# Kernel tuning notes

Measured on AMD Instinct MI355X. Metric: run time of the kernel, lower is better.

Reference implementation:

```python
import jax, jax.numpy as jnp
import numpy as np

DIM = 256
CTX_DIM = 256
HEADS = 32
DIM_HEAD = 32
INNER = HEADS * DIM_HEAD


def mish(x):
    return x * jnp.tanh(jax.nn.softplus(x))


def setup_inputs() -> dict:
    key = jax.random.key(0)
    ks = jax.random.split(key, 16)
    B, Lq, Lp = 16, 128, 512
    s = 0.02
    return {
        "x": jax.random.normal(ks[0], (B * Lq, DIM), jnp.float32),
        "context": jax.random.normal(ks[1], (B * Lp, CTX_DIM), jnp.float32),
        "batch_dis": jax.random.normal(ks[2], (B, Lp, Lq, 3), jnp.float32),
        "batch_dis_emb": jax.random.normal(ks[3], (B, Lp, Lq, HEADS), jnp.float32),
        "protein_len": Lp,
        "ligand_len": Lq,
        # params ([in, out] layout, torch Linear transposed)
        "W_qk": jax.random.normal(ks[4], (DIM, INNER), jnp.float32) * s,
        "W_v": jax.random.normal(ks[5], (DIM, INNER), jnp.float32) * s,
        "W_cqk": jax.random.normal(ks[6], (CTX_DIM, INNER), jnp.float32) * s,
        "W_cv": jax.random.normal(ks[7], (CTX_DIM, INNER), jnp.float32) * s,
        "W_m1": jax.random.normal(ks[8], (2 * HEADS, 4 * HEADS), jnp.float32) * s,
        "W_m2": jax.random.normal(ks[9], (4 * HEADS, 2 * HEADS), jnp.float32) * s,
        "b_m2": jnp.zeros((2 * HEADS,), jnp.float32),
        "W_o": jax.random.normal(ks[10], (INNER, DIM), jnp.float32) * s,
        "b_o": jnp.zeros((DIM,), jnp.float32),
        "W_d1": jax.random.normal(ks[11], (HEADS, 2 * HEADS), jnp.float32) * s,
        "b_d1": jnp.zeros((2 * HEADS,), jnp.float32),
        "W_d2": jax.random.normal(ks[12], (2 * HEADS, HEADS), jnp.float32) * s,
        "b_d2": jnp.zeros((HEADS,), jnp.float32),
    }


def reference(x, context, batch_dis, batch_dis_emb, protein_len, ligand_len,
              W_qk, W_v, W_cqk, W_cv, W_m1, W_m2, b_m2, W_o, b_o,
              W_d1, b_d1, W_d2, b_d2):
    h, dh = HEADS, DIM_HEAD
    scale = dh ** -0.5
    B = x.shape[0] // ligand_len
    # projections; split heads: [B, L, h, dh]
    qk = (x @ W_qk).reshape(B, ligand_len, h, dh)
    cqk = (context @ W_cqk).reshape(B, protein_len, h, dh)
    cv = (context @ W_cv).reshape(B, protein_len, h, dh)
    # ligand->protein attention scores: [B, h, Lq, Lp]
    sim = jnp.einsum('bihd,bjhd->bhij', qk, cqk) * scale
    # distance-embedding channels: [B, Lp, Lq, h] -> [B, h, Lq, Lp]
    dis = jnp.transpose(batch_dis_emb, (0, 3, 2, 1))
    s = jnp.concatenate([sim, dis], axis=1)           # [B, 2h, Lq, Lp]
    s = jnp.moveaxis(s, 1, -1)                        # [B, Lq, Lp, 2h]
    s = mish(s @ W_m1) @ W_m2 + b_m2                  # attn_mlp over channel dim
    attn = jax.nn.softmax(s, axis=2)                  # softmax over protein (j)
    # first h heads attend into context values
    out = jnp.einsum('bijh,bjhd->bihd', attn[..., :h], cv)
    out = out.reshape(B * ligand_len, h * dh) @ W_o + b_o   # [N_lig, dim]
    # last h heads aggregate 3D distance vectors
    out_dis = jnp.einsum('bijh,bjid->bidh', attn[..., h:], batch_dis)
    out_dis = out_dis.reshape(B * ligand_len, 3, h)
    out_dis = mish(out_dis @ W_d1 + b_d1) @ W_d2 + b_d2      # [N_lig, 3, h]
    return out, out_dis
```

## Files before the change

### kernel.cpp

```cpp
#include <hip/hip_runtime.h>

typedef unsigned short u16;
typedef unsigned int   u32;
typedef __attribute__((ext_vector_type(8))) short bf16x8;
typedef __attribute__((ext_vector_type(4))) float f32x4;

#define MFMA_BF16 __builtin_amdgcn_mfma_f32_16x16x32_bf16

__device__ __forceinline__ float bf2f(u16 v) {
    u32 x = ((u32)v) << 16;
    return __builtin_bit_cast(float, x);
}
__device__ __forceinline__ float bflo(u32 u) { return __builtin_bit_cast(float, u << 16); }
__device__ __forceinline__ float bfhi(u32 u) { return __builtin_bit_cast(float, u & 0xffff0000u); }
__device__ __forceinline__ u16 f2bf(float f) {
    u32 x = __builtin_bit_cast(u32, f);
    u32 r = (x + 0x7fffu + ((x >> 16) & 1u)) >> 16;
    return (u16)r;
}
__device__ __forceinline__ float mishf(float x) {
    float p = 1.f + __expf(x);
    float q = p * p;
    float r = (q - 1.f) / (q + 1.f);
    return (x > 20.f) ? x : x * r;
}

__global__ __launch_bounds__(256) void gemm_mfma(
    const float* __restrict__ A, const float* __restrict__ W, u16* __restrict__ C,
    int M, int N, int K, float scale)
{
    __shared__ u16 As[128 * 40];
    __shared__ u16 Bf[4 * 64 * 8];

    const int tid = threadIdx.x;
    const int lane = tid & 63, wv = tid >> 6;
    const int qd = lane >> 4, ln = lane & 15;
    const int m0 = blockIdx.y * 128, n0 = blockIdx.x * 64;

    f32x4 acc[2][4];
#pragma unroll
    for (int a = 0; a < 2; ++a)
#pragma unroll
        for (int nt = 0; nt < 4; ++nt) acc[a][nt] = (f32x4){0.f, 0.f, 0.f, 0.f};

    for (int k0 = 0; k0 < K; k0 += 32) {
        {
            int r = tid >> 1, kh = (tid & 1) * 16;
            const float* ap = A + (size_t)(m0 + r) * K + k0 + kh;
            float4 a0 = ((const float4*)ap)[0];
            float4 a1 = ((const float4*)ap)[1];
            float4 a2 = ((const float4*)ap)[2];
            float4 a3 = ((const float4*)ap)[3];
            uint4 p0, p1;
            p0.x = (u32)f2bf(a0.x) | ((u32)f2bf(a0.y) << 16);
            p0.y = (u32)f2bf(a0.z) | ((u32)f2bf(a0.w) << 16);
            p0.z = (u32)f2bf(a1.x) | ((u32)f2bf(a1.y) << 16);
            p0.w = (u32)f2bf(a1.z) | ((u32)f2bf(a1.w) << 16);
            p1.x = (u32)f2bf(a2.x) | ((u32)f2bf(a2.y) << 16);
            p1.y = (u32)f2bf(a2.z) | ((u32)f2bf(a2.w) << 16);
            p1.z = (u32)f2bf(a3.x) | ((u32)f2bf(a3.y) << 16);
            p1.w = (u32)f2bf(a3.z) | ((u32)f2bf(a3.w) << 16);
            *(uint4*)&As[r * 40 + kh]     = p0;
            *(uint4*)&As[r * 40 + kh + 8] = p1;
        }
        {
            int nt = tid >> 6, q = (tid >> 4) & 3, nn = tid & 15;
            const float* wp = W + (size_t)(k0 + q * 8) * N + n0 + nt * 16 + nn;
            bf16x8 v;
#pragma unroll
            for (int j = 0; j < 8; ++j) v[j] = (short)f2bf(wp[(size_t)j * N]);
            *(bf16x8*)&Bf[tid * 8] = v;
        }
        __syncthreads();
        bf16x8 af0 = *(const bf16x8*)&As[(wv * 32 + ln) * 40 + qd * 8];
        bf16x8 af1 = *(const bf16x8*)&As[(wv * 32 + 16 + ln) * 40 + qd * 8];
#pragma unroll
        for (int nt = 0; nt < 4; ++nt) {
            bf16x8 bfr = *(const bf16x8*)&Bf[(nt * 64 + lane) * 8];
            acc[0][nt] = MFMA_BF16(af0, bfr, acc[0][nt], 0, 0, 0);
            acc[1][nt] = MFMA_BF16(af1, bfr, acc[1][nt], 0, 0, 0);
        }
        __syncthreads();
    }
#pragma unroll
    for (int a = 0; a < 2; ++a)
#pragma unroll
        for (int nt = 0; nt < 4; ++nt)
#pragma unroll
            for (int r = 0; r < 4; ++r)
                C[(size_t)(m0 + wv * 32 + a * 16 + qd * 4 + r) * N + n0 + nt * 16 + ln] =
                    f2bf(acc[a][nt][r] * scale);
}

__global__ __launch_bounds__(256) void transpose_cv(
    const u16* __restrict__ cv, u16* __restrict__ cvT)
{
    __shared__ u16 T[64 * 80];
    const int tid = threadIdx.x;
    const int ct = blockIdx.x * 64, jt = blockIdx.y * 64, b = blockIdx.z;
    {
        int j_l = tid >> 2, seg = tid & 3;
        const u16* src = cv + (size_t)(b * 512 + jt + j_l) * 1024 + ct + seg * 16;
        uint4 v0 = ((const uint4*)src)[0];
        uint4 v1 = ((const uint4*)src)[1];
        u16* tp = &T[seg * 16 * 80 + j_l];
        tp[0*80] = (u16)(v0.x & 0xffff); tp[1*80] = (u16)(v0.x >> 16);
        tp[2*80] = (u16)(v0.y & 0xffff); tp[3*80] = (u16)(v0.y >> 16);
        tp[4*80] = (u16)(v0.z & 0xffff); tp[5*80] = (u16)(v0.z >> 16);
        tp[6*80] = (u16)(v0.w & 0xffff); tp[7*80] = (u16)(v0.w >> 16);
        tp[8*80] = (u16)(v1.x & 0xffff); tp[9*80] = (u16)(v1.x >> 16);
        tp[10*80] = (u16)(v1.y & 0xffff); tp[11*80] = (u16)(v1.y >> 16);
        tp[12*80] = (u16)(v1.z & 0xffff); tp[13*80] = (u16)(v1.z >> 16);
        tp[14*80] = (u16)(v1.w & 0xffff); tp[15*80] = (u16)(v1.w >> 16);
    }
    __syncthreads();
    {
        int ch_l = tid >> 2, sg = tid & 3;
        u16* dst = cvT + (size_t)(b * 1024 + ct + ch_l) * 512 + jt + sg * 16;
        ((uint4*)dst)[0] = *(const uint4*)&T[ch_l * 80 + sg * 16];
        ((uint4*)dst)[1] = *(const uint4*)&T[ch_l * 80 + sg * 16 + 8];
    }
}

__global__ __launch_bounds__(256) void prep(
    const float* __restrict__ Wo, const float* __restrict__ W1, const float* __restrict__ W2,
    u16* __restrict__ WoT, u16* __restrict__ w1b, u16* __restrict__ w2b)
{
    const int bb = blockIdx.x, t = threadIdx.x;
    if (bb < 256) {
#pragma unroll
        for (int kk = 0; kk < 4; ++kk)
            WoT[(size_t)t * 1024 + bb * 4 + kk] = f2bf(Wo[(size_t)(bb * 4 + kk) * 256 + t]);
    } else {
        for (int u = 0; u < 32; ++u) {
            int idx = t + 256 * u;
            int j = idx & 7, lane = (idx >> 3) & 63, f = idx >> 9;
            int n = lane & 15, q = lane >> 4, ntc = f & 7, ks = f >> 3;
            w1b[idx] = f2bf(W1[(ks * 32 + q * 8 + j) * 128 + ntc * 16 + n]);
        }
        for (int u = 0; u < 32; ++u) {
            int idx = t + 256 * u;
            int j = idx & 7, lane = (idx >> 3) & 63, f = idx >> 9;
            int n = lane & 15, q = lane >> 4, ot = f & 3, ks = f >> 2;
            w2b[idx] = f2bf(W2[(ks * 32 + q * 8 + j) * 64 + ot * 16 + n]);
        }
    }
}

__global__ __launch_bounds__(256, 1) void attn5(
    const u16* __restrict__ qk,
    const u16* __restrict__ cqk,
    const u16* __restrict__ cvT,
    const float* __restrict__ bde,
    const float* __restrict__ bdis,
    const u16* __restrict__ w1b, const u16* __restrict__ w2b,
    const float* __restrict__ b2,
    float* __restrict__ partial)
{
    __shared__ __align__(16) char smem[62976];
    u16*   ES  = (u16*)smem;
    u16*   MT  = (u16*)(smem + 20480);
    float* BD  = (float*)(smem + 25600);
    u16*   EST = (u16*)(smem + 29696);
    u16*   W1B = (u16*)(smem + 54784);

    const int tid = threadIdx.x;
    const int lane = tid & 63, wv = tid >> 6;
    const int qd = lane >> 4, ln = lane & 15;
    const int nblk = blockIdx.x;
    const int xcd = nblk & 7, g = nblk >> 3;
    const int b = xcd * 2 + (g & 1);
    const int r2 = g >> 1;
    const int it = r2 >> 2, jq = r2 & 3;
    const int i0 = it * 16;
    const int pidx = (b * 8 + it) * 4 + jq;

    for (int k = tid; k < 4096; k += 256) ((u32*)W1B)[k] = ((const u32*)w1b)[k];

    float b2r[4];
#pragma unroll
    for (int ot = 0; ot < 4; ++ot) b2r[ot] = b2[ot * 16 + ln];

    bf16x8 qkf[8];
#pragma unroll
    for (int hh = 0; hh < 8; ++hh) {
        int h = wv * 8 + hh;
        qkf[hh] = *(const bf16x8*)(qk + ((size_t)(b * 128 + i0 + ln)) * 1024 + h * 32 + qd * 8);
    }

    f32x4 oacc[8][2];
#pragma unroll
    for (int a = 0; a < 8; ++a)
#pragma unroll
        for (int c = 0; c < 2; ++c) oacc[a][c] = (f32x4){0.f, 0.f, 0.f, 0.f};
    float dn[4][4] = {};
    float dd[4][3][2] = {};

    __syncthreads();

#pragma clang loop unroll(disable)
    for (int ps = 0; ps < 8; ++ps) {
        const int jg0 = jq * 128 + ps * 16;

        {
            const u16* crow = cqk + (size_t)(b * 512 + jg0 + ln) * 1024 + qd * 8;
#pragma unroll
            for (int hh = 0; hh < 4; ++hh) {
                const int h0 = wv * 8 + hh * 2;
                bf16x8 b0 = *(const bf16x8*)(crow + h0 * 32);
                bf16x8 b1 = *(const bf16x8*)(crow + (h0 + 1) * 32);
                f32x4 c0 = (f32x4){0.f, 0.f, 0.f, 0.f}, c1 = c0;
                c0 = MFMA_BF16(qkf[hh * 2],     b0, c0, 0, 0, 0);
                c1 = MFMA_BF16(qkf[hh * 2 + 1], b1, c1, 0, 0, 0);
#pragma unroll
                for (int r = 0; r < 4; ++r) {
                    u32 pv = (u32)f2bf(c0[r]) | ((u32)f2bf(c1[r]) << 16);
                    *(u32*)&ES[((qd * 4 + r) * 16 + ln) * 40 + h0] = pv;
                }
            }
        }
        {
            int ii = tid & 15, jj = tid >> 4;
            const float* sp = bdis + ((size_t)(b * 512 + jg0 + jj) * 128 + i0 + ii) * 3;
            float* dp2 = &BD[(ii * 16 + jj) * 4];
            dp2[0] = sp[0]; dp2[1] = sp[1]; dp2[2] = sp[2];
        }
        __syncthreads();

#pragma unroll
        for (int s = 0; s < 4; ++s) {
            const int i_loc = wv * 4 + s;
            bf16x8 af0 = *(const bf16x8*)&ES[(i_loc * 16 + ln) * 40 + qd * 8];
            bf16x8 af1;
            {
                const float* dp = bde + (((size_t)(b * 512 + jg0 + ln)) * 128 + i0 + i_loc) * 32 + qd * 8;
                float4 a0 = ((const float4*)dp)[0];
                float4 a1 = ((const float4*)dp)[1];
                af1[0] = (short)f2bf(a0.x); af1[1] = (short)f2bf(a0.y);
                af1[2] = (short)f2bf(a0.z); af1[3] = (short)f2bf(a0.w);
                af1[4] = (short)f2bf(a1.x); af1[5] = (short)f2bf(a1.y);
                af1[6] = (short)f2bf(a1.z); af1[7] = (short)f2bf(a1.w);
            }
            f32x4 uacc[4];
#pragma unroll
            for (int ot = 0; ot < 4; ++ot) uacc[ot] = (f32x4){0.f, 0.f, 0.f, 0.f};
            u16* mt = MT + wv * 640;
#pragma unroll
            for (int cg = 0; cg < 4; ++cg) {
                bf16x8 w00 = *(const bf16x8*)&W1B[((cg * 2 + 0) * 64 + lane) * 8];
                bf16x8 w01 = *(const bf16x8*)&W1B[((cg * 2 + 1) * 64 + lane) * 8];
                bf16x8 w10 = *(const bf16x8*)&W1B[((8 + cg * 2 + 0) * 64 + lane) * 8];
                bf16x8 w11 = *(const bf16x8*)&W1B[((8 + cg * 2 + 1) * 64 + lane) * 8];
                f32x4 t0 = (f32x4){0.f, 0.f, 0.f, 0.f}, t1 = t0;
                t0 = MFMA_BF16(af0, w00, t0, 0, 0, 0);
                t0 = MFMA_BF16(af1, w10, t0, 0, 0, 0);
                t1 = MFMA_BF16(af0, w01, t1, 0, 0, 0);
                t1 = MFMA_BF16(af1, w11, t1, 0, 0, 0);
#pragma unroll
                for (int r = 0; r < 4; ++r) {
                    mt[(qd * 4 + r) * 40 + ln]      = f2bf(mishf(t0[r]));
                    mt[(qd * 4 + r) * 40 + 16 + ln] = f2bf(mishf(t1[r]));
                }
                bf16x8 ta = *(const bf16x8*)&mt[ln * 40 + qd * 8];
#pragma unroll
                for (int ot = 0; ot < 4; ++ot) {
                    bf16x8 wf = *(const bf16x8*)(w2b + ((size_t)(cg * 4 + ot) * 64 + lane) * 8);
                    uacc[ot] = MFMA_BF16(ta, wf, uacc[ot], 0, 0, 0);
                }
            }
            float Ev[4][4];
#pragma unroll
            for (int ot = 0; ot < 4; ++ot) {
#pragma unroll
                for (int r = 0; r < 4; ++r) Ev[ot][r] = __expf(uacc[ot][r] + b2r[ot]);
                dn[s][ot] += Ev[ot][0] + Ev[ot][1] + Ev[ot][2] + Ev[ot][3];
            }
#pragma unroll
            for (int r = 0; r < 4; ++r) {
                const float* bp = &BD[(i_loc * 16 + qd * 4 + r) * 4];
#pragma unroll
                for (int d = 0; d < 3; ++d) {
                    dd[s][d][0] += Ev[2][r] * bp[d];
                    dd[s][d][1] += Ev[3][r] * bp[d];
                }
            }
#pragma unroll
            for (int ot = 0; ot < 2; ++ot) {
                const int base = (ot * 16 + ln) * 392 + i_loc * 24 + qd * 4;
                *(u32*)&EST[base]     = (u32)f2bf(Ev[ot][0]) | ((u32)f2bf(Ev[ot][1]) << 16);
                *(u32*)&EST[base + 2] = (u32)f2bf(Ev[ot][2]) | ((u32)f2bf(Ev[ot][3]) << 16);
            }
        }
        __syncthreads();

#pragma unroll
        for (int hh = 0; hh < 8; ++hh) {
            const int h = wv * 8 + hh;
            bf16x8 af = (bf16x8){0, 0, 0, 0, 0, 0, 0, 0};
            if (qd < 2) af = *(const bf16x8*)&EST[h * 392 + ln * 24 + qd * 8];
#pragma unroll
            for (int nt = 0; nt < 2; ++nt) {
                bf16x8 bfr = (bf16x8){0, 0, 0, 0, 0, 0, 0, 0};
                if (qd < 2)
                    bfr = *(const bf16x8*)(cvT + ((size_t)(b * 1024 + h * 32 + nt * 16 + ln)) * 512 + jg0 + qd * 8);
                oacc[hh][nt] = MFMA_BF16(af, bfr, oacc[hh][nt], 0, 0, 0);
            }
        }
        __syncthreads();
    }

    float* P = partial + (size_t)pidx * 18944;
#pragma unroll
    for (int hh = 0; hh < 8; ++hh)
#pragma unroll
        for (int nt = 0; nt < 2; ++nt)
#pragma unroll
            for (int r = 0; r < 4; ++r)
                P[(size_t)(qd * 4 + r) * 1024 + (wv * 8 + hh) * 32 + nt * 16 + ln] = oacc[hh][nt][r];
#pragma unroll
    for (int s = 0; s < 4; ++s)
#pragma unroll
        for (int ot = 0; ot < 4; ++ot) {
            float v = dn[s][ot];
            v += __shfl_xor(v, 16, 64);
            v += __shfl_xor(v, 32, 64);
            if (qd == 0) P[16384 + (wv * 4 + s) * 64 + ot * 16 + ln] = v;
        }
#pragma unroll
    for (int s = 0; s < 4; ++s)
#pragma unroll
        for (int d = 0; d < 3; ++d)
#pragma unroll
            for (int o = 0; o < 2; ++o) {
                float v = dd[s][d][o];
                v += __shfl_xor(v, 16, 64);
                v += __shfl_xor(v, 32, 64);
                if (qd == 0) P[17408 + (wv * 4 + s) * 96 + d * 32 + o * 16 + ln] = v;
            }
}

__global__ __launch_bounds__(256, 2) void finalize(
    const float* __restrict__ partial, const u16* __restrict__ WoT,
    const float* __restrict__ bo,
    const float* __restrict__ Wd1, const float* __restrict__ bd1,
    const float* __restrict__ Wd2, const float* __restrict__ bd2,
    float* __restrict__ out0, float* __restrict__ out1)
{
    __shared__ float denomL[1024];
    __shared__ u16 preL[16 * 1032];
    __shared__ float odisL[1536];
    __shared__ float r1L[3072];

    const int tid = threadIdx.x;
    const int f = blockIdx.x;
    const int b = f >> 3, it = f & 7;
    const int row0 = b * 128 + it * 16;
    const float* P0 = partial + (size_t)(f * 4 + 0) * 18944;
    const float* P1 = partial + (size_t)(f * 4 + 1) * 18944;
    const float* P2 = partial + (size_t)(f * 4 + 2) * 18944;
    const float* P3 = partial + (size_t)(f * 4 + 3) * 18944;

    for (int k = tid; k < 1024; k += 256)
        denomL[k] = P0[16384 + k] + P1[16384 + k] + P2[16384 + k] + P3[16384 + k];
    __syncthreads();

    {
        const int h = tid >> 3;
#pragma unroll
        for (int i = 0; i < 16; ++i) {
            float4 a = *(const float4*)&P0[(size_t)i * 1024 + tid * 4];
            float4 bq = *(const float4*)&P1[(size_t)i * 1024 + tid * 4];
            float4 c = *(const float4*)&P2[(size_t)i * 1024 + tid * 4];
            float4 d = *(const float4*)&P3[(size_t)i * 1024 + tid * 4];
            float rdn = 1.f / denomL[i * 64 + h];
            u32 p0 = (u32)f2bf((a.x + bq.x + c.x + d.x) * rdn) | ((u32)f2bf((a.y + bq.y + c.y + d.y) * rdn) << 16);
            u32 p1 = (u32)f2bf((a.z + bq.z + c.z + d.z) * rdn) | ((u32)f2bf((a.w + bq.w + c.w + d.w) * rdn) << 16);
            *(uint2*)(void*)&preL[i * 1032 + tid * 4] = make_uint2(p0, p1);
        }
    }
    for (int idx = tid; idx < 1536; idx += 256) {
        int i = idx / 96, rm = idx % 96, h = rm & 31;
        odisL[idx] = (P0[17408 + idx] + P1[17408 + idx] + P2[17408 + idx] + P3[17408 + idx])
                     / denomL[i * 64 + 32 + h];
    }
    __syncthreads();

    {
        const int lane = tid & 63, wv = tid >> 6;
        const int qd = lane >> 4, ln = lane & 15;
        f32x4 acc[4];
#pragma unroll
        for (int nt = 0; nt < 4; ++nt) acc[nt] = (f32x4){0.f, 0.f, 0.f, 0.f};
#pragma clang loop unroll(disable)
        for (int ks = 0; ks < 32; ++ks) {
            bf16x8 af = *(const bf16x8*)&preL[ln * 1032 + ks * 32 + qd * 8];
#pragma unroll
            for (int nt = 0; nt < 4; ++nt) {
                bf16x8 wf = *(const bf16x8*)(WoT + ((size_t)(wv * 64 + nt * 16 + ln)) * 1024 + ks * 32 + qd * 8);
                acc[nt] = MFMA_BF16(af, wf, acc[nt], 0, 0, 0);
            }
        }
#pragma unroll
        for (int nt = 0; nt < 4; ++nt) {
            int col = wv * 64 + nt * 16 + ln;
            float bv = bo[col];
#pragma unroll
            for (int r = 0; r < 4; ++r)
                out0[(size_t)(row0 + qd * 4 + r) * 256 + col] = acc[nt][r] + bv;
        }
    }

    for (int idx = tid; idx < 3072; idx += 256) {
        int i = idx / 192, rm = idx % 192, d = rm / 64, c = rm & 63;
        float t = bd1[c];
#pragma unroll
        for (int hh = 0; hh < 32; ++hh)
            t += odisL[i * 96 + d * 32 + hh] * Wd1[hh * 64 + c];
        r1L[idx] = mishf(t);
    }
    __syncthreads();
    for (int idx = tid; idx < 1536; idx += 256) {
        int i = idx / 96, rm = idx % 96, d = rm >> 5, h = rm & 31;
        float v = bd2[h];
#pragma unroll
        for (int c = 0; c < 64; ++c)
            v += r1L[i * 192 + d * 64 + c] * Wd2[c * 32 + h];
        out1[(size_t)(row0 + i) * 96 + d * 32 + h] = v;
    }
}

extern "C" void kernel_launch(void* const* d_in, const int* in_sizes, int n_in,
                              void* d_out, int out_size, void* d_ws, size_t ws_size,
                              hipStream_t stream) {
    const float* x    = (const float*)d_in[0];
    const float* ctx  = (const float*)d_in[1];
    const float* bdis = (const float*)d_in[2];
    const float* bde  = (const float*)d_in[3];
    const float* Wqk  = (const float*)d_in[6];
    const float* Wcqk = (const float*)d_in[8];
    const float* Wcv  = (const float*)d_in[9];
    const float* Wm1  = (const float*)d_in[10];
    const float* Wm2  = (const float*)d_in[11];
    const float* bm2  = (const float*)d_in[12];
    const float* Wo   = (const float*)d_in[13];
    const float* bo   = (const float*)d_in[14];
    const float* Wd1  = (const float*)d_in[15];
    const float* bd1  = (const float*)d_in[16];
    const float* Wd2  = (const float*)d_in[17];
    const float* bd2  = (const float*)d_in[18];

    char* ws = (char*)d_ws;
    u16* qk_ws  = (u16*)(ws);
    u16* cqk_ws = (u16*)(ws + 4194304);
    u16* cvT_ws = (u16*)(ws + 20971520);
    u16* w1b    = (u16*)(ws + 37748736);
    u16* w2b    = (u16*)(ws + 37765120);
    u16* WoT    = (u16*)(ws + 37781504);
    float* part = (float*)(ws + 38305792);
    u16* cv_rm  = (u16*)(ws + 38305792);

    float* out0 = (float*)d_out;
    float* out1 = out0 + (size_t)2048 * 256;

    const float SCALE = 0.17677669529663687f;

    prep<<<257, 256, 0, stream>>>(Wo, Wm1, Wm2, WoT, w1b, w2b);
    gemm_mfma<<<dim3(16, 16), 256, 0, stream>>>(x,   Wqk,  qk_ws,  2048, 1024, 256, SCALE);
    gemm_mfma<<<dim3(16, 64), 256, 0, stream>>>(ctx, Wcqk, cqk_ws, 8192, 1024, 256, 1.0f);
    gemm_mfma<<<dim3(16, 64), 256, 0, stream>>>(ctx, Wcv,  cv_rm,  8192, 1024, 256, 1.0f);
    transpose_cv<<<dim3(16, 8, 16), 256, 0, stream>>>(cv_rm, cvT_ws);
    attn5<<<512, 256, 0, stream>>>(qk_ws, cqk_ws, cvT_ws, bde, bdis, w1b, w2b, bm2, part);
    finalize<<<128, 256, 0, stream>>>(part, WoT, bo, Wd1, bd1, Wd2, bd2, out0, out1);
}
```

Measured before the change: 562.5 us.

## Use packed bf16 conversion and exp2 intrinsics with log2e folded into weights

Replaces the software round-to-nearest bf16 conversion with the hardware v_cvt_pk_bf16_f32 instruction across the GEMM, attention and reduction kernels. Mish is rewritten with raw v_exp_f32 and v_rcp_f32 plus FMAs in place of the division. The log2e factor is folded into W2 and b2 so the softmax exponent becomes a single exp2, and W2's channel order is permuted so mish outputs can be written as packed pairs. Distance loads move to float4 shared-memory accesses. The aim is fewer ALU instructions in the VALU-heavy attention loop, at the cost of dropping the x>20 guard in mish, which could overflow to inf/NaN for large inputs.

Result: slower. 577.3 us (+2.6%).

```diff
diff --git a/kernel.cpp b/kernel.cpp
--- a/kernel.cpp
+++ b/kernel.cpp
@@ -6,23 +6,34 @@
 typedef __attribute__((ext_vector_type(4))) float f32x4;
 
 #define MFMA_BF16 __builtin_amdgcn_mfma_f32_16x16x32_bf16
-
-__device__ __forceinline__ float bf2f(u16 v) {
-    u32 x = ((u32)v) << 16;
-    return __builtin_bit_cast(float, x);
-}
-__device__ __forceinline__ float bflo(u32 u) { return __builtin_bit_cast(float, u << 16); }
-__device__ __forceinline__ float bfhi(u32 u) { return __builtin_bit_cast(float, u & 0xffff0000u); }
+#define LOG2E 1.4426950408889634f
+
 __device__ __forceinline__ u16 f2bf(float f) {
     u32 x = __builtin_bit_cast(u32, f);
     u32 r = (x + 0x7fffu + ((x >> 16) & 1u)) >> 16;
     return (u16)r;
 }
+__device__ __forceinline__ u32 cvt_pk_bf16(float lo, float hi) {
+    u32 r;
+    asm("v_cvt_pk_bf16_f32 %0, %1, %2" : "=v"(r) : "v"(lo), "v"(hi));
+    return r;
+}
+__device__ __forceinline__ float exp2_asm(float x) {
+    float r;
+    asm("v_exp_f32 %0, %1" : "=v"(r) : "v"(x));
+    return r;
+}
+__device__ __forceinline__ float rcp_asm(float x) {
+    float r;
+    asm("v_rcp_f32 %0, %1" : "=v"(r) : "v"(x));
+    return r;
+}
 __device__ __forceinline__ float mishf(float x) {
-    float p = 1.f + __expf(x);
-    float q = p * p;
-    float r = (q - 1.f) / (q + 1.f);
-    return (x > 20.f) ? x : x * r;
+    float e = exp2_asm(x * LOG2E);
+    float p = 1.f + e;
+    float d = __builtin_fmaf(p, p, 1.f);
+    float r = __builtin_fmaf(-2.f, rcp_asm(d), 1.f);
+    return x * r;
 }
 
 __global__ __launch_bounds__(256) void gemm_mfma(
@@ -52,24 +63,28 @@
             float4 a2 = ((const float4*)ap)[2];
             float4 a3 = ((const float4*)ap)[3];
             uint4 p0, p1;
-            p0.x = (u32)f2bf(a0.x) | ((u32)f2bf(a0.y) << 16);
-            p0.y = (u32)f2bf(a0.z) | ((u32)f2bf(a0.w) << 16);
-            p0.z = (u32)f2bf(a1.x) | ((u32)f2bf(a1.y) << 16);
-            p0.w = (u32)f2bf(a1.z) | ((u32)f2bf(a1.w) << 16);
-            p1.x = (u32)f2bf(a2.x) | ((u32)f2bf(a2.y) << 16);
-            p1.y = (u32)f2bf(a2.z) | ((u32)f2bf(a2.w) << 16);
-            p1.z = (u32)f2bf(a3.x) | ((u32)f2bf(a3.y) << 16);
-            p1.w = (u32)f2bf(a3.z) | ((u32)f2bf(a3.w) << 16);
+            p0.x = cvt_pk_bf16(a0.x, a0.y);
+            p0.y = cvt_pk_bf16(a0.z, a0.w);
+            p0.z = cvt_pk_bf16(a1.x, a1.y);
+            p0.w = cvt_pk_bf16(a1.z, a1.w);
+            p1.x = cvt_pk_bf16(a2.x, a2.y);
+            p1.y = cvt_pk_bf16(a2.z, a2.w);
+            p1.z = cvt_pk_bf16(a3.x, a3.y);
+            p1.w = cvt_pk_bf16(a3.z, a3.w);
             *(uint4*)&As[r * 40 + kh]     = p0;
             *(uint4*)&As[r * 40 + kh + 8] = p1;
         }
         {
             int nt = tid >> 6, q = (tid >> 4) & 3, nn = tid & 15;
             const float* wp = W + (size_t)(k0 + q * 8) * N + n0 + nt * 16 + nn;
-            bf16x8 v;
-#pragma unroll
-            for (int j = 0; j < 8; ++j) v[j] = (short)f2bf(wp[(size_t)j * N]);
-            *(bf16x8*)&Bf[tid * 8] = v;
+            float w0 = wp[0], w1 = wp[(size_t)1 * N], w2 = wp[(size_t)2 * N], w3 = wp[(size_t)3 * N];
+            float w4 = wp[(size_t)4 * N], w5 = wp[(size_t)5 * N], w6 = wp[(size_t)6 * N], w7 = wp[(size_t)7 * N];
+            uint4 u;
+            u.x = cvt_pk_bf16(w0, w1);
+            u.y = cvt_pk_bf16(w2, w3);
+            u.z = cvt_pk_bf16(w4, w5);
+            u.w = cvt_pk_bf16(w6, w7);
+            *(uint4*)&Bf[tid * 8] = u;
         }
         __syncthreads();
         bf16x8 af0 = *(const bf16x8*)&As[(wv * 32 + ln) * 40 + qd * 8];
@@ -85,11 +100,15 @@
 #pragma unroll
     for (int a = 0; a < 2; ++a)
 #pragma unroll
-        for (int nt = 0; nt < 4; ++nt)
-#pragma unroll
-            for (int r = 0; r < 4; ++r)
-                C[(size_t)(m0 + wv * 32 + a * 16 + qd * 4 + r) * N + n0 + nt * 16 + ln] =
-                    f2bf(acc[a][nt][r] * scale);
+        for (int nt = 0; nt < 4; ++nt) {
+            u32 pk0 = cvt_pk_bf16(acc[a][nt][0] * scale, acc[a][nt][1] * scale);
+            u32 pk1 = cvt_pk_bf16(acc[a][nt][2] * scale, acc[a][nt][3] * scale);
+            size_t base = (size_t)(m0 + wv * 32 + a * 16 + qd * 4) * N + n0 + nt * 16 + ln;
+            C[base]               = (u16)pk0;
+            C[base + (size_t)N]   = (u16)(pk0 >> 16);
+            C[base + (size_t)2*N] = (u16)pk1;
+            C[base + (size_t)3*N] = (u16)(pk1 >> 16);
+        }
 }
 
 __global__ __launch_bounds__(256) void transpose_cv(
@@ -142,7 +161,9 @@
             int idx = t + 256 * u;
             int j = idx & 7, lane = (idx >> 3) & 63, f = idx >> 9;
             int n = lane & 15, q = lane >> 4, ot = f & 3, ks = f >> 2;
-            w2b[idx] = f2bf(W2[(ks * 32 + q * 8 + j) * 64 + ot * 16 + n]);
+            int k = q * 8 + j;
+            int ch = ((k & 1) << 4) | (k >> 1);
+            w2b[idx] = f2bf(W2[(ks * 32 + ch) * 64 + ot * 16 + n] * LOG2E);
         }
     }
 }
@@ -179,7 +200,7 @@
 
     float b2r[4];
 #pragma unroll
-    for (int ot = 0; ot < 4; ++ot) b2r[ot] = b2[ot * 16 + ln];
+    for (int ot = 0; ot < 4; ++ot) b2r[ot] = b2[ot * 16 + ln] * LOG2E;
 
     bf16x8 qkf[8];
 #pragma unroll
@@ -213,17 +234,16 @@
                 c0 = MFMA_BF16(qkf[hh * 2],     b0, c0, 0, 0, 0);
                 c1 = MFMA_BF16(qkf[hh * 2 + 1], b1, c1, 0, 0, 0);
 #pragma unroll
-                for (int r = 0; r < 4; ++r) {
-                    u32 pv = (u32)f2bf(c0[r]) | ((u32)f2bf(c1[r]) << 16);
-                    *(u32*)&ES[((qd * 4 + r) * 16 + ln) * 40 + h0] = pv;
-                }
+                for (int r = 0; r < 4; ++r)
+                    *(u32*)&ES[((qd * 4 + r) * 16 + ln) * 40 + h0] = cvt_pk_bf16(c0[r], c1[r]);
             }
         }
         {
             int ii = tid & 15, jj = tid >> 4;
             const float* sp = bdis + ((size_t)(b * 512 + jg0 + jj) * 128 + i0 + ii) * 3;
-            float* dp2 = &BD[(ii * 16 + jj) * 4];
-            dp2[0] = sp[0]; dp2[1] = sp[1]; dp2[2] = sp[2];
+            float4 v4;
+            v4.x = sp[0]; v4.y = sp[1]; v4.z = sp[2]; v4.w = 0.f;
+            *(float4*)&BD[(ii * 16 + jj) * 4] = v4;
         }
         __syncthreads();
 
@@ -236,10 +256,12 @@
                 const float* dp = bde + (((size_t)(b * 512 + jg0 + ln)) * 128 + i0 + i_loc) * 32 + qd * 8;
                 float4 a0 = ((const float4*)dp)[0];
                 float4 a1 = ((const float4*)dp)[1];
-                af1[0] = (short)f2bf(a0.x); af1[1] = (short)f2bf(a0.y);
-                af1[2] = (short)f2bf(a0.z); af1[3] = (short)f2bf(a0.w);
-                af1[4] = (short)f2bf(a1.x); af1[5] = (short)f2bf(a1.y);
-                af1[6] = (short)f2bf(a1.z); af1[7] = (short)f2bf(a1.w);
+                uint4 u;
+                u.x = cvt_pk_bf16(a0.x, a0.y);
+                u.y = cvt_pk_bf16(a0.z, a0.w);
+                u.z = cvt_pk_bf16(a1.x, a1.y);
+                u.w = cvt_pk_bf16(a1.z, a1.w);
+                af1 = __builtin_bit_cast(bf16x8, u);
             }
             f32x4 uacc[4];
 #pragma unroll
@@ -258,8 +280,8 @@
                 t1 = MFMA_BF16(af1, w11, t1, 0, 0, 0);
 #pragma unroll
                 for (int r = 0; r < 4; ++r) {
-                    mt[(qd * 4 + r) * 40 + ln]      = f2bf(mishf(t0[r]));
-                    mt[(qd * 4 + r) * 40 + 16 + ln] = f2bf(mishf(t1[r]));
+                    u32 pk = cvt_pk_bf16(mishf(t0[r]), mishf(t1[r]));
+                    *(u32*)&mt[(qd * 4 + r) * 40 + (ln << 1)] = pk;
                 }
                 bf16x8 ta = *(const bf16x8*)&mt[ln * 40 + qd * 8];
 #pragma unroll
@@ -272,23 +294,21 @@
 #pragma unroll
             for (int ot = 0; ot < 4; ++ot) {
 #pragma unroll
-                for (int r = 0; r < 4; ++r) Ev[ot][r] = __expf(uacc[ot][r] + b2r[ot]);
-                dn[s][ot] += Ev[ot][0] + Ev[ot][1] + Ev[ot][2] + Ev[ot][3];
+                for (int r = 0; r < 4; ++r) Ev[ot][r] = exp2_asm(uacc[ot][r] + b2r[ot]);
+                dn[s][ot] += (Ev[ot][0] + Ev[ot][1]) + (Ev[ot][2] + Ev[ot][3]);
             }
 #pragma unroll
             for (int r = 0; r < 4; ++r) {
-                const float* bp = &BD[(i_loc * 16 + qd * 4 + r) * 4];
-#pragma unroll
-                for (int d = 0; d < 3; ++d) {
-                    dd[s][d][0] += Ev[2][r] * bp[d];
-                    dd[s][d][1] += Ev[3][r] * bp[d];
-                }
+                float4 bp = *(const float4*)&BD[(i_loc * 16 + qd * 4 + r) * 4];
+                dd[s][0][0] += Ev[2][r] * bp.x; dd[s][0][1] += Ev[3][r] * bp.x;
+                dd[s][1][0] += Ev[2][r] * bp.y; dd[s][1][1] += Ev[3][r] * bp.y;
+                dd[s][2][0] += Ev[2][r] * bp.z; dd[s][2][1] += Ev[3][r] * bp.z;
             }
 #pragma unroll
             for (int ot = 0; ot < 2; ++ot) {
                 const int base = (ot * 16 + ln) * 392 + i_loc * 24 + qd * 4;
-                *(u32*)&EST[base]     = (u32)f2bf(Ev[ot][0]) | ((u32)f2bf(Ev[ot][1]) << 16);
-                *(u32*)&EST[base + 2] = (u32)f2bf(Ev[ot][2]) | ((u32)f2bf(Ev[ot][3]) << 16);
+                *(u32*)&EST[base]     = cvt_pk_bf16(Ev[ot][0], Ev[ot][1]);
+                *(u32*)&EST[base + 2] = cvt_pk_bf16(Ev[ot][2], Ev[ot][3]);
             }
         }
         __syncthreads();
@@ -373,8 +393,8 @@
             float4 c = *(const float4*)&P2[(size_t)i * 1024 + tid * 4];
             float4 d = *(const float4*)&P3[(size_t)i * 1024 + tid * 4];
             float rdn = 1.f / denomL[i * 64 + h];
-            u32 p0 = (u32)f2bf((a.x + bq.x + c.x + d.x) * rdn) | ((u32)f2bf((a.y + bq.y + c.y + d.y) * rdn) << 16);
-            u32 p1 = (u32)f2bf((a.z + bq.z + c.z + d.z) * rdn) | ((u32)f2bf((a.w + bq.w + c.w + d.w) * rdn) << 16);
+            u32 p0 = cvt_pk_bf16((a.x + bq.x + c.x + d.x) * rdn, (a.y + bq.y + c.y + d.y) * rdn);
+            u32 p1 = cvt_pk_bf16((a.z + bq.z + c.z + d.z) * rdn, (a.w + bq.w + c.w + d.w) * rdn);
             *(uint2*)(void*)&preL[i * 1032 + tid * 4] = make_uint2(p0, p1);
         }
     }
```
